# Kernel tuning notes

Hardware: AMD Instinct MI355X
Metric: run time of the kernel (lower is better)

## Reference

```python
import jax, jax.numpy as jnp
import numpy as np


def log_g(x):
    # log(relu(x) + 0.5) for x >= 0, else -softplus(-x)
    pos = jnp.log(jnp.maximum(x, 0.0) + 0.5)
    neg = -jax.nn.softplus(-x)
    return jnp.where(x >= 0, pos, neg)


def parallel_scan_log(log_coeffs, log_values):
    # h_t = a_t * h_{t-1} + b_t, computed stably in log space
    a_star = jnp.cumsum(log_coeffs, axis=1)
    log_h0_plus_b_star = jax.lax.cumlogsumexp(log_values - a_star, axis=1)
    log_h = a_star + log_h0_plus_b_star
    return jnp.exp(log_h)


def setup_inputs() -> dict:
    key = jax.random.key(0)
    k1, k2 = jax.random.split(key)
    B, S, D = 8, 4096, 1024
    x = jax.random.normal(k1, (B, S, D), dtype=jnp.float32)
    # torch nn.Linear(dim, 2*inner_dim, bias=False): weight [2*inner_dim, dim]
    W_hg = jax.random.normal(k2, (2 * D, D), dtype=jnp.float32) * (1.0 / np.sqrt(D))
    return {"x": x, "W_hg": W_hg}


def reference(x, W_hg):
    # hidden_gate projection: [B,S,D] @ [D, 2*inner] -> [B,S,2*inner]
    hg = jnp.einsum("bsd,ed->bse", x, W_hg)
    hidden, gate = jnp.split(hg, 2, axis=-1)
    log_coeffs = -jax.nn.softplus(gate)       # log(1 - z)
    log_z = -jax.nn.softplus(-gate)           # log(z)
    log_tilde_h = log_g(hidden)
    log_values = log_z + log_tilde_h
    out = parallel_scan_log(log_coeffs, log_values)
    # expansion_factor == 1.0 -> self.out is Identity; dropout_prob == 0 -> Identity
    return out
```

## Files before the change

### kernel.cpp

```cpp
#include <hip/hip_runtime.h>

#define B_   8
#define S_   4096
#define D_   1024
#define M_   (B_ * S_)
#define N_   (2 * D_)
#define K_   D_
#define CCH  128
#define LCH  32

#define BK   32
#define NT   (K_ / BK)

typedef __attribute__((ext_vector_type(8))) short bf16x8;
typedef __attribute__((ext_vector_type(4))) float f32x4;

__device__ __forceinline__ unsigned short f2bf(float f) {
  union { float f; unsigned u; } v; v.f = f;
  unsigned u = v.u;
  u = u + 0x7fffu + ((u >> 16) & 1u);
  return (unsigned short)(u >> 16);
}
__device__ __forceinline__ float bf2f(unsigned short h) {
  union { unsigned u; float f; } v; v.u = ((unsigned)h) << 16;
  return v.f;
}
__device__ __forceinline__ float sigmoidf_(float x) {
  return 1.0f / (1.0f + __expf(-x));
}

#define GLL(src, dst) __builtin_amdgcn_global_load_lds(                     \
      (const __attribute__((address_space(1))) void*)(src),                 \
      (__attribute__((address_space(3))) void*)(dst), 16, 0, 0)

__global__ __launch_bounds__(256) void k_cvt2(const float* __restrict__ x,
                                              const float* __restrict__ W,
                                              unsigned short* __restrict__ xb,
                                              unsigned short* __restrict__ wb) {
  const int n4x = (M_ * K_) / 4;
  const int n4t = n4x + (N_ * K_) / 4;
  int i = blockIdx.x * 256 + threadIdx.x;
  const int stride = gridDim.x * 256;
  for (; i < n4t; i += stride) {
    const float4* src = (i < n4x) ? &reinterpret_cast<const float4*>(x)[i]
                                  : &reinterpret_cast<const float4*>(W)[i - n4x];
    float4 v = *src;
    ushort4 o;
    o.x = f2bf(v.x); o.y = f2bf(v.y); o.z = f2bf(v.z); o.w = f2bf(v.w);
    if (i < n4x) reinterpret_cast<ushort4*>(xb)[i] = o;
    else         reinterpret_cast<ushort4*>(wb)[i - n4x] = o;
  }
}

__global__ __launch_bounds__(512, 4) void k_gemm(const unsigned short* __restrict__ xb,
                                                 const unsigned short* __restrict__ wb,
                                                 unsigned short* __restrict__ HLp,
                                                 unsigned short* __restrict__ APp) {
  __shared__ unsigned short lds[36864];
  const int tid = threadIdx.x;
  int wg = blockIdx.x;
  wg = (wg & 7) * 256 + (wg >> 3);
  const int bm = wg >> 4;
  const int bn = wg & 15;
  const int lane = tid & 63;
  const int wid = tid >> 6;
  const int wrr = wid >> 1;
  const int wcc = wid & 1;
  const int fr = lane & 15;
  const int hi = lane >> 4;

  const int srow = tid >> 2;
  const int scol = ((tid & 3) ^ ((srow >> 1) & 3)) * 16;
  const char* aS = (const char*)xb + (size_t)(bm * 256 + srow) * 2048 + scol;
  const char* bS = (const char*)wb +
      (size_t)(bn * 64 + srow + ((srow >= 64) ? 960 : 0)) * 2048 + scol;
  char* const ldsc = (char*)lds + (size_t)tid * 16;
  const char* const ldsr = (const char*)lds;

  const int sA = ((hi ^ ((fr >> 1) & 3)) * 16);
  const int arow  = (wrr * 64 + fr) * 64;
  const int browH = 16384 + (wcc * 32 + fr) * 64;
  const int browG = browH + 4096;

  f32x4 accH[4][2] = {};
  f32x4 accG[4][2] = {};
  bf16x8 av[4], bvH[2], bvG[2];

  GLL(aS,               ldsc);
  GLL(aS + 262144,      ldsc + 8192);
  GLL(bS,               ldsc + 16384);
  GLL(aS + 64,          ldsc + 24576);
  GLL(aS + 262144 + 64, ldsc + 32768);
  GLL(bS + 64,          ldsc + 40960);
  asm volatile("s_waitcnt vmcnt(3)\n\ts_barrier" ::: "memory");

  int sl = 0;
  int sn = 49152;

  for (int t = 0; t < NT; ++t) {
    const bool st2 = (t < NT - 2);
    if (st2) {
      const size_t kb = (size_t)(t + 2) * 64;
      char* dq = ldsc + sn;
      GLL(aS + kb,          dq);
      GLL(aS + 262144 + kb, dq + 8192);
      GLL(bS + kb,          dq + 16384);
    }
    const char* Ab = ldsr + sl;
#pragma unroll
    for (int m = 0; m < 4; ++m)
      av[m] = *(const bf16x8*)(Ab + arow + m * 1024 + sA);
#pragma unroll
    for (int n = 0; n < 2; ++n) {
      bvH[n] = *(const bf16x8*)(Ab + browH + n * 1024 + sA);
      bvG[n] = *(const bf16x8*)(Ab + browG + n * 1024 + sA);
    }
    __builtin_amdgcn_s_setprio(1);
#pragma unroll
    for (int m = 0; m < 4; ++m) {
#pragma unroll
      for (int n = 0; n < 2; ++n) {
        accH[m][n] = __builtin_amdgcn_mfma_f32_16x16x32_bf16(av[m], bvH[n], accH[m][n], 0, 0, 0);
        accG[m][n] = __builtin_amdgcn_mfma_f32_16x16x32_bf16(av[m], bvG[n], accG[m][n], 0, 0, 0);
      }
    }
    __builtin_amdgcn_s_setprio(0);
    if (st2) asm volatile("s_waitcnt vmcnt(3)\n\ts_barrier" ::: "memory");
    else     asm volatile("s_waitcnt vmcnt(0)\n\ts_barrier" ::: "memory");
    sl += 24576; if (sl == 73728) sl = 0;
    sn += 24576; if (sn == 73728) sn = 0;
  }

  const int dcol0 = bn * 64 + wcc * 32 + fr;
  const size_t rowg0 = (size_t)(bm * 256 + wrr * 64);
#pragma unroll
  for (int kap = 0; kap < 2; ++kap) {
#pragma unroll
    for (int n = 0; n < 2; ++n) {
      float a_[2][4], b_[2][4];
#pragma unroll
      for (int mm = 0; mm < 2; ++mm)
#pragma unroll
        for (int i = 0; i < 4; ++i) {
          float zg = sigmoidf_(accG[kap * 2 + mm][n][i]);
          float hv = accH[kap * 2 + mm][n][i];
          float gg = (hv >= 0.f) ? (hv + 0.5f) : sigmoidf_(hv);
          a_[mm][i] = 1.f - zg;
          b_[mm][i] = zg * gg;
        }
      float A1 = a_[0][0] * a_[0][1] * a_[0][2] * a_[0][3];
      float B1 = ((b_[0][0] * a_[0][1] + b_[0][1]) * a_[0][2] + b_[0][2]) * a_[0][3] + b_[0][3];
      float A2 = a_[1][0] * a_[1][1] * a_[1][2] * a_[1][3];
      float B2 = ((b_[1][0] * a_[1][1] + b_[1][1]) * a_[1][2] + b_[1][2]) * a_[1][3] + b_[1][3];
      float Ai = A1, Bi = B1;
      { float Ao = __shfl(Ai, (lane - 16) & 63), Bo = __shfl(Bi, (lane - 16) & 63);
        if (hi >= 1) { Bi += Ai * Bo; Ai *= Ao; } }
      { float Ao = __shfl(Ai, (lane - 32) & 63), Bo = __shfl(Bi, (lane - 32) & 63);
        if (hi >= 2) { Bi += Ai * Bo; Ai *= Ao; } }
      float Ae1 = __shfl(Ai, (lane - 16) & 63), Be1 = __shfl(Bi, (lane - 16) & 63);
      if (hi == 0) { Ae1 = 1.f; Be1 = 0.f; }
      float At = __shfl(Ai, fr + 48), Bt = __shfl(Bi, fr + 48);
      float Ai2 = A2, Bi2 = B2;
      { float Ao = __shfl(Ai2, (lane - 16) & 63), Bo = __shfl(Bi2, (lane - 16) & 63);
        if (hi >= 1) { Bi2 += Ai2 * Bo; Ai2 *= Ao; } }
      { float Ao = __shfl(Ai2, (lane - 32) & 63), Bo = __shfl(Bi2, (lane - 32) & 63);
        if (hi >= 2) { Bi2 += Ai2 * Bo; Ai2 *= Ao; } }
      float Ae2 = __shfl(Ai2, (lane - 16) & 63), Be2 = __shfl(Bi2, (lane - 16) & 63);
      if (hi == 0) { Ae2 = 1.f; Be2 = 0.f; }
      const float Ax2 = Ae2 * At;
      const float Bx2 = Be2 + Ae2 * Bt;
      const int d = dcol0 + n * 16;
      size_t rr = (rowg0 + kap * 32 + hi * 4) * 1024 + d;
      float ap = Ae1, hl = Be1;
#pragma unroll
      for (int i = 0; i < 4; ++i) {
        hl = a_[0][i] * hl + b_[0][i]; ap *= a_[0][i];
        HLp[rr] = f2bf(hl);
        APp[rr] = f2bf(ap);
        rr += 1024;
      }
      rr = (rowg0 + kap * 32 + 16 + hi * 4) * 1024 + d;
      ap = Ax2; hl = Bx2;
#pragma unroll
      for (int i = 0; i < 4; ++i) {
        hl = a_[1][i] * hl + b_[1][i]; ap *= a_[1][i];
        HLp[rr] = f2bf(hl);
        APp[rr] = f2bf(ap);
        rr += 1024;
      }
    }
  }
}

__global__ __launch_bounds__(256) void k_scan2(unsigned short* __restrict__ HL,
                                               const unsigned short* __restrict__ AP) {
  const int gid = blockIdx.x * 256 + threadIdx.x;
  const int b = gid >> 8;
  const int d0 = (gid & 255) << 2;
  float c0 = 0.f, c1 = 0.f, c2 = 0.f, c3 = 0.f;
  for (int c = 0; c < CCH; ++c) {
    size_t off = ((size_t)b * S_ + (size_t)c * LCH + 31) * 1024 + d0;
    ushort4 hu = *reinterpret_cast<const ushort4*>(HL + off);
    ushort4 au = *reinterpret_cast<const ushort4*>(AP + off);
    c0 = fmaf(bf2f(au.x), c0, bf2f(hu.x));
    c1 = fmaf(bf2f(au.y), c1, bf2f(hu.y));
    c2 = fmaf(bf2f(au.z), c2, bf2f(hu.z));
    c3 = fmaf(bf2f(au.w), c3, bf2f(hu.w));
    ushort4 o; o.x = f2bf(c0); o.y = f2bf(c1); o.z = f2bf(c2); o.w = f2bf(c3);
    *reinterpret_cast<ushort4*>(HL + off) = o;
  }
}

__global__ __launch_bounds__(256) void k_scan3(const unsigned short* __restrict__ HL,
                                               const unsigned short* __restrict__ AP,
                                               float* __restrict__ out) {
  const int gid = blockIdx.x * 256 + threadIdx.x;
  const int c = blockIdx.y;
  const int b = gid >> 8;
  const int d0 = (gid & 255) << 2;
  const size_t rbase = (size_t)b * S_ + (size_t)c * LCH;
  float4 carry = {0.f, 0.f, 0.f, 0.f};
  if (c > 0) {
    ushort4 cu = *reinterpret_cast<const ushort4*>(HL + (rbase - 1) * 1024 + d0);
    carry.x = bf2f(cu.x); carry.y = bf2f(cu.y); carry.z = bf2f(cu.z); carry.w = bf2f(cu.w);
  }
  size_t off = rbase * 1024 + d0;
#pragma unroll 8
  for (int s = 0; s < LCH - 1; ++s) {
    ushort4 hu = *reinterpret_cast<const ushort4*>(HL + off);
    ushort4 au = *reinterpret_cast<const ushort4*>(AP + off);
    float4 o;
    o.x = fmaf(bf2f(au.x), carry.x, bf2f(hu.x));
    o.y = fmaf(bf2f(au.y), carry.y, bf2f(hu.y));
    o.z = fmaf(bf2f(au.z), carry.z, bf2f(hu.z));
    o.w = fmaf(bf2f(au.w), carry.w, bf2f(hu.w));
    *reinterpret_cast<float4*>(out + off) = o;
    off += 1024;
  }
  ushort4 hu = *reinterpret_cast<const ushort4*>(HL + off);
  float4 o;
  o.x = bf2f(hu.x); o.y = bf2f(hu.y); o.z = bf2f(hu.z); o.w = bf2f(hu.w);
  *reinterpret_cast<float4*>(out + off) = o;
}

extern "C" void kernel_launch(void* const* d_in, const int* in_sizes, int n_in,
                              void* d_out, int out_size, void* d_ws, size_t ws_size,
                              hipStream_t stream) {
  const float* x = (const float*)d_in[0];
  const float* W = (const float*)d_in[1];
  float* out = (float*)d_out;

  unsigned char* w = (unsigned char*)d_ws;
  unsigned short* xb  = (unsigned short*)(w);
  unsigned short* wb  = (unsigned short*)(w + 67108864);
  unsigned short* HLp = (unsigned short*)(w + 71303168);
  unsigned short* APp = (unsigned short*)(w + 138412032);

  k_cvt2<<<4096, 256, 0, stream>>>(x, W, xb, wb);
  k_gemm<<<(M_ / 256) * 16, 512, 0, stream>>>(xb, wb, HLp, APp);
  k_scan2<<<8, 256, 0, stream>>>(HLp, APp);
  k_scan3<<<dim3(8, CCH), 256, 0, stream>>>(HLp, APp, out);
}
```

Measured before the change: 288.2 us.

## Fuse fp32-to-bf16 conversion of x into GEMM loads and keep chunk carries in fp32

The GEMM now reads fp32 activations straight from global memory into registers, converts them to bf16 and writes them to LDS, which removes the separate conversion pass over x and its bf16 copy in the workspace. Weights are still converted by a smaller kernel. Chunk totals are also written as fp32 into compact arrays that the carry scan reads and turns into per-chunk carry-ins. This avoids bf16 rounding of the carries and strided reads of the large buffers. The cost is register-staged A loads with double-buffered float4 registers inside the GEMM, which raises register pressure and adds conversion work to the main loop.

```diff
diff --git a/kernel.cpp b/kernel.cpp
--- a/kernel.cpp
+++ b/kernel.cpp
@@ -1,4 +1,5 @@
 #include <hip/hip_runtime.h>
+#include <hip/hip_bf16.h>
 
 #define B_   8
 #define S_   4096
@@ -28,34 +29,36 @@
 __device__ __forceinline__ float sigmoidf_(float x) {
   return 1.0f / (1.0f + __expf(-x));
 }
+__device__ __forceinline__ unsigned short bfu(float f) {
+  __hip_bfloat16 h = __float2bfloat16(f);
+  return *reinterpret_cast<unsigned short*>(&h);
+}
+__device__ __forceinline__ bf16x8 pk8(float4 a, float4 b) {
+  union { bf16x8 v; unsigned short u[8]; } r;
+  r.u[0] = bfu(a.x); r.u[1] = bfu(a.y); r.u[2] = bfu(a.z); r.u[3] = bfu(a.w);
+  r.u[4] = bfu(b.x); r.u[5] = bfu(b.y); r.u[6] = bfu(b.z); r.u[7] = bfu(b.w);
+  return r.v;
+}
 
 #define GLL(src, dst) __builtin_amdgcn_global_load_lds(                     \
       (const __attribute__((address_space(1))) void*)(src),                 \
       (__attribute__((address_space(3))) void*)(dst), 16, 0, 0)
 
-__global__ __launch_bounds__(256) void k_cvt2(const float* __restrict__ x,
-                                              const float* __restrict__ W,
-                                              unsigned short* __restrict__ xb,
+__global__ __launch_bounds__(256) void k_cvtw(const float* __restrict__ W,
                                               unsigned short* __restrict__ wb) {
-  const int n4x = (M_ * K_) / 4;
-  const int n4t = n4x + (N_ * K_) / 4;
-  int i = blockIdx.x * 256 + threadIdx.x;
-  const int stride = gridDim.x * 256;
-  for (; i < n4t; i += stride) {
-    const float4* src = (i < n4x) ? &reinterpret_cast<const float4*>(x)[i]
-                                  : &reinterpret_cast<const float4*>(W)[i - n4x];
-    float4 v = *src;
-    ushort4 o;
-    o.x = f2bf(v.x); o.y = f2bf(v.y); o.z = f2bf(v.z); o.w = f2bf(v.w);
-    if (i < n4x) reinterpret_cast<ushort4*>(xb)[i] = o;
-    else         reinterpret_cast<ushort4*>(wb)[i - n4x] = o;
-  }
-}
-
-__global__ __launch_bounds__(512, 4) void k_gemm(const unsigned short* __restrict__ xb,
+  const int i = blockIdx.x * 256 + threadIdx.x;
+  float4 v = reinterpret_cast<const float4*>(W)[i];
+  ushort4 o;
+  o.x = f2bf(v.x); o.y = f2bf(v.y); o.z = f2bf(v.z); o.w = f2bf(v.w);
+  reinterpret_cast<ushort4*>(wb)[i] = o;
+}
+
+__global__ __launch_bounds__(512, 4) void k_gemm(const float* __restrict__ xf,
                                                  const unsigned short* __restrict__ wb,
                                                  unsigned short* __restrict__ HLp,
-                                                 unsigned short* __restrict__ APp) {
+                                                 unsigned short* __restrict__ APp,
+                                                 float* __restrict__ Atot,
+                                                 float* __restrict__ Btot) {
   __shared__ unsigned short lds[36864];
   const int tid = threadIdx.x;
   int wg = blockIdx.x;
@@ -70,10 +73,10 @@
   const int hi = lane >> 4;
 
   const int srow = tid >> 2;
-  const int scol = ((tid & 3) ^ ((srow >> 1) & 3)) * 16;
-  const char* aS = (const char*)xb + (size_t)(bm * 256 + srow) * 2048 + scol;
+  const int sblk = (tid & 3) ^ ((srow >> 1) & 3);
+  const char* aSf = (const char*)xf + (size_t)(bm * 256 + srow) * 4096 + sblk * 32;
   const char* bS = (const char*)wb +
-      (size_t)(bn * 64 + srow + ((srow >= 64) ? 960 : 0)) * 2048 + scol;
+      (size_t)(bn * 64 + srow + ((srow >= 64) ? 960 : 0)) * 2048 + sblk * 16;
   char* const ldsc = (char*)lds + (size_t)tid * 16;
   const char* const ldsr = (const char*)lds;
 
@@ -85,51 +88,72 @@
   f32x4 accH[4][2] = {};
   f32x4 accG[4][2] = {};
   bf16x8 av[4], bvH[2], bvG[2];
-
-  GLL(aS,               ldsc);
-  GLL(aS + 262144,      ldsc + 8192);
-  GLL(bS,               ldsc + 16384);
-  GLL(aS + 64,          ldsc + 24576);
-  GLL(aS + 262144 + 64, ldsc + 32768);
-  GLL(bS + 64,          ldsc + 40960);
-  asm volatile("s_waitcnt vmcnt(3)\n\ts_barrier" ::: "memory");
+  float4 e0, e1, e2, e3, o0, o1, o2, o3;
 
   int sl = 0;
-  int sn = 49152;
-
-  for (int t = 0; t < NT; ++t) {
-    const bool st2 = (t < NT - 2);
-    if (st2) {
-      const size_t kb = (size_t)(t + 2) * 64;
-      char* dq = ldsc + sn;
-      GLL(aS + kb,          dq);
-      GLL(aS + 262144 + kb, dq + 8192);
-      GLL(bS + kb,          dq + 16384);
-    }
-    const char* Ab = ldsr + sl;
-#pragma unroll
-    for (int m = 0; m < 4; ++m)
-      av[m] = *(const bf16x8*)(Ab + arow + m * 1024 + sA);
-#pragma unroll
-    for (int n = 0; n < 2; ++n) {
-      bvH[n] = *(const bf16x8*)(Ab + browH + n * 1024 + sA);
-      bvG[n] = *(const bf16x8*)(Ab + browG + n * 1024 + sA);
-    }
-    __builtin_amdgcn_s_setprio(1);
-#pragma unroll
-    for (int m = 0; m < 4; ++m) {
-#pragma unroll
-      for (int n = 0; n < 2; ++n) {
-        accH[m][n] = __builtin_amdgcn_mfma_f32_16x16x32_bf16(av[m], bvH[n], accH[m][n], 0, 0, 0);
-        accG[m][n] = __builtin_amdgcn_mfma_f32_16x16x32_bf16(av[m], bvG[n], accG[m][n], 0, 0, 0);
-      }
-    }
-    __builtin_amdgcn_s_setprio(0);
-    if (st2) asm volatile("s_waitcnt vmcnt(3)\n\ts_barrier" ::: "memory");
-    else     asm volatile("s_waitcnt vmcnt(0)\n\ts_barrier" ::: "memory");
-    sl += 24576; if (sl == 73728) sl = 0;
-    sn += 24576; if (sn == 73728) sn = 0;
-  }
+  int sn1 = 24576;
+  int sn2 = 49152;
+
+  GLL(bS, ldsc + 16384);
+  e0 = *(const float4*)(aSf);
+  e1 = *(const float4*)(aSf + 16);
+  e2 = *(const float4*)(aSf + 524288);
+  e3 = *(const float4*)(aSf + 524288 + 16);
+  asm volatile("" ::: "memory");
+  GLL(bS + 64, ldsc + 40960);
+  o0 = *(const float4*)(aSf + 128);
+  o1 = *(const float4*)(aSf + 128 + 16);
+  o2 = *(const float4*)(aSf + 524288 + 128);
+  o3 = *(const float4*)(aSf + 524288 + 128 + 16);
+  asm volatile("s_waitcnt vmcnt(5)" ::: "memory");
+  *(bf16x8*)(ldsc)        = pk8(e0, e1);
+  *(bf16x8*)(ldsc + 8192) = pk8(e2, e3);
+  asm volatile("s_waitcnt lgkmcnt(0)\n\ts_barrier" ::: "memory");
+
+#define TILE(T, I0, I1, I2, I3, W0, W1, W2, W3)                               \
+  {                                                                           \
+    const int t_ = (T);                                                       \
+    if (t_ < NT - 2) {                                                        \
+      const size_t kb = (size_t)(t_ + 2) * 128;                               \
+      GLL(bS + (size_t)(t_ + 2) * 64, ldsc + sn2 + 16384);                    \
+      I0 = *(const float4*)(aSf + kb);                                        \
+      I1 = *(const float4*)(aSf + kb + 16);                                   \
+      I2 = *(const float4*)(aSf + kb + 524288);                               \
+      I3 = *(const float4*)(aSf + kb + 524288 + 16);                          \
+    }                                                                         \
+    const char* Ab = ldsr + sl;                                               \
+    _Pragma("unroll") for (int m = 0; m < 4; ++m)                             \
+      av[m] = *(const bf16x8*)(Ab + arow + m * 1024 + sA);                    \
+    _Pragma("unroll") for (int n = 0; n < 2; ++n) {                           \
+      bvH[n] = *(const bf16x8*)(Ab + browH + n * 1024 + sA);                  \
+      bvG[n] = *(const bf16x8*)(Ab + browG + n * 1024 + sA);                  \
+    }                                                                         \
+    __builtin_amdgcn_s_setprio(1);                                            \
+    _Pragma("unroll") for (int m = 0; m < 4; ++m)                             \
+      _Pragma("unroll") for (int n = 0; n < 2; ++n) {                         \
+        accH[m][n] = __builtin_amdgcn_mfma_f32_16x16x32_bf16(av[m], bvH[n],   \
+                                                             accH[m][n], 0, 0, 0); \
+        accG[m][n] = __builtin_amdgcn_mfma_f32_16x16x32_bf16(av[m], bvG[n],   \
+                                                             accG[m][n], 0, 0, 0); \
+      }                                                                       \
+    __builtin_amdgcn_s_setprio(0);                                            \
+    if (t_ < NT - 2)       asm volatile("s_waitcnt vmcnt(5)" ::: "memory");   \
+    else if (t_ == NT - 2) asm volatile("s_waitcnt vmcnt(0)" ::: "memory");   \
+    if (t_ < NT - 1) {                                                        \
+      *(bf16x8*)(ldsc + sn1)        = pk8(W0, W1);                            \
+      *(bf16x8*)(ldsc + sn1 + 8192) = pk8(W2, W3);                            \
+      asm volatile("s_waitcnt lgkmcnt(0)\n\ts_barrier" ::: "memory");         \
+    }                                                                         \
+    sl += 24576;  if (sl == 73728) sl = 0;                                    \
+    sn1 += 24576; if (sn1 == 73728) sn1 = 0;                                  \
+    sn2 += 24576; if (sn2 == 73728) sn2 = 0;                                  \
+  }
+
+  for (int tt = 0; tt < NT / 2; ++tt) {
+    TILE(2 * tt,     e0, e1, e2, e3, o0, o1, o2, o3);
+    TILE(2 * tt + 1, o0, o1, o2, o3, e0, e1, e2, e3);
+  }
+#undef TILE
 
   const int dcol0 = bn * 64 + wcc * 32 + fr;
   const size_t rowg0 = (size_t)(bm * 256 + wrr * 64);
@@ -188,45 +212,44 @@
         APp[rr] = f2bf(ap);
         rr += 1024;
       }
+      if (hi == 3) {
+        const int rg = (int)rowg0 + kap * 32;
+        const size_t ci = (size_t)((rg >> 5) & 127) * 8192 + (size_t)(rg >> 12) * 1024 + d;
+        Atot[ci] = ap;
+        Btot[ci] = hl;
+      }
     }
   }
 }
 
-__global__ __launch_bounds__(256) void k_scan2(unsigned short* __restrict__ HL,
-                                               const unsigned short* __restrict__ AP) {
+__global__ __launch_bounds__(256) void k_scan2(const float* __restrict__ Atot,
+                                               const float* __restrict__ Btot,
+                                               float* __restrict__ Cin) {
   const int gid = blockIdx.x * 256 + threadIdx.x;
-  const int b = gid >> 8;
-  const int d0 = (gid & 255) << 2;
-  float c0 = 0.f, c1 = 0.f, c2 = 0.f, c3 = 0.f;
+  float4 carry = {0.f, 0.f, 0.f, 0.f};
   for (int c = 0; c < CCH; ++c) {
-    size_t off = ((size_t)b * S_ + (size_t)c * LCH + 31) * 1024 + d0;
-    ushort4 hu = *reinterpret_cast<const ushort4*>(HL + off);
-    ushort4 au = *reinterpret_cast<const ushort4*>(AP + off);
-    c0 = fmaf(bf2f(au.x), c0, bf2f(hu.x));
-    c1 = fmaf(bf2f(au.y), c1, bf2f(hu.y));
-    c2 = fmaf(bf2f(au.z), c2, bf2f(hu.z));
-    c3 = fmaf(bf2f(au.w), c3, bf2f(hu.w));
-    ushort4 o; o.x = f2bf(c0); o.y = f2bf(c1); o.z = f2bf(c2); o.w = f2bf(c3);
-    *reinterpret_cast<ushort4*>(HL + off) = o;
+    reinterpret_cast<float4*>(Cin)[(size_t)c * 2048 + gid] = carry;
+    float4 a  = reinterpret_cast<const float4*>(Atot)[(size_t)c * 2048 + gid];
+    float4 bt = reinterpret_cast<const float4*>(Btot)[(size_t)c * 2048 + gid];
+    carry.x = fmaf(a.x, carry.x, bt.x);
+    carry.y = fmaf(a.y, carry.y, bt.y);
+    carry.z = fmaf(a.z, carry.z, bt.z);
+    carry.w = fmaf(a.w, carry.w, bt.w);
   }
 }
 
 __global__ __launch_bounds__(256) void k_scan3(const unsigned short* __restrict__ HL,
                                                const unsigned short* __restrict__ AP,
+                                               const float* __restrict__ Cin,
                                                float* __restrict__ out) {
   const int gid = blockIdx.x * 256 + threadIdx.x;
   const int c = blockIdx.y;
   const int b = gid >> 8;
   const int d0 = (gid & 255) << 2;
-  const size_t rbase = (size_t)b * S_ + (size_t)c * LCH;
-  float4 carry = {0.f, 0.f, 0.f, 0.f};
-  if (c > 0) {
-    ushort4 cu = *reinterpret_cast<const ushort4*>(HL + (rbase - 1) * 1024 + d0);
-    carry.x = bf2f(cu.x); carry.y = bf2f(cu.y); carry.z = bf2f(cu.z); carry.w = bf2f(cu.w);
-  }
-  size_t off = rbase * 1024 + d0;
+  float4 carry = reinterpret_cast<const float4*>(Cin)[(size_t)c * 2048 + gid];
+  size_t off = ((size_t)b * S_ + (size_t)c * LCH) * 1024 + d0;
 #pragma unroll 8
-  for (int s = 0; s < LCH - 1; ++s) {
+  for (int s = 0; s < LCH; ++s) {
     ushort4 hu = *reinterpret_cast<const ushort4*>(HL + off);
     ushort4 au = *reinterpret_cast<const ushort4*>(AP + off);
     float4 o;
@@ -237,10 +260,6 @@
     *reinterpret_cast<float4*>(out + off) = o;
     off += 1024;
   }
-  ushort4 hu = *reinterpret_cast<const ushort4*>(HL + off);
-  float4 o;
-  o.x = bf2f(hu.x); o.y = bf2f(hu.y); o.z = bf2f(hu.z); o.w = bf2f(hu.w);
-  *reinterpret_cast<float4*>(out + off) = o;
 }
 
 extern "C" void kernel_launch(void* const* d_in, const int* in_sizes, int n_in,
@@ -251,13 +270,15 @@
   float* out = (float*)d_out;
 
   unsigned char* w = (unsigned char*)d_ws;
-  unsigned short* xb  = (unsigned short*)(w);
-  unsigned short* wb  = (unsigned short*)(w + 67108864);
-  unsigned short* HLp = (unsigned short*)(w + 71303168);
-  unsigned short* APp = (unsigned short*)(w + 138412032);
-
-  k_cvt2<<<4096, 256, 0, stream>>>(x, W, xb, wb);
-  k_gemm<<<(M_ / 256) * 16, 512, 0, stream>>>(xb, wb, HLp, APp);
-  k_scan2<<<8, 256, 0, stream>>>(HLp, APp);
-  k_scan3<<<dim3(8, CCH), 256, 0, stream>>>(HLp, APp, out);
-}
+  unsigned short* wb   = (unsigned short*)(w);
+  unsigned short* HLp  = (unsigned short*)(w + 4194304);
+  unsigned short* APp  = (unsigned short*)(w + 71303168);
+  float* Atot = (float*)(w + 138412032);
+  float* Btot = (float*)(w + 142606336);
+  float* Cin  = (float*)(w + 146800640);
+
+  k_cvtw<<<2048, 256, 0, stream>>>(W, wb);
+  k_gemm<<<(M_ / 256) * 16, 512, 0, stream>>>(x, wb, HLp, APp, Atot, Btot);
+  k_scan2<<<8, 256, 0, stream>>>(Atot, Btot, Cin);
+  k_scan3<<<dim3(8, CCH), 256, 0, stream>>>(HLp, APp, Cin, out);
+}
```

Result: slower. 690.8 us (+139.7%).
